# Optimization experiments

Measured on AMD Instinct MI355X. Metric: run time of the kernel, lower is better.

The kernel has to match this reference:

```python
import jax, jax.numpy as jnp
import numpy as np

QUERY_DIM, KEY_DIM, N_BATCH, N_KEYS = 512, 256, 2048, 512

def setup_inputs() -> dict:
    key = jax.random.key(0)
    k1, k2, k3, k4, k5, k6 = jax.random.split(key, 6)
    queries = jax.random.normal(k1, (N_BATCH, QUERY_DIM), dtype=jnp.float32)
    keys = jax.random.normal(k2, (N_BATCH, N_KEYS, KEY_DIM), dtype=jnp.float32)
    trans_keys = jax.random.normal(k3, (N_BATCH, N_KEYS, KEY_DIM), dtype=jnp.float32)
    null_mask = jax.random.randint(k4, (N_BATCH, N_KEYS), 0, 2).astype(jnp.bool_)
    # nn.Linear(query_dim, key_dim) params
    bound = 1.0 / np.sqrt(QUERY_DIM)
    W = jax.random.uniform(k5, (KEY_DIM, QUERY_DIM), dtype=jnp.float32, minval=-bound, maxval=bound)
    b = jax.random.uniform(k6, (KEY_DIM,), dtype=jnp.float32, minval=-bound, maxval=bound)
    return {"queries": queries, "keys": keys, "trans_keys": trans_keys,
            "null_mask": null_mask, "W": W, "b": b}

def reference(queries, keys, trans_keys, null_mask, W, b):
    # trans_queries = linear_in(queries): (B, key_dim)
    trans_queries = queries @ W.T + b
    # alpha = bmm(keys, trans_queries[:, :, None]).squeeze(2): (B, n_keys)
    alpha = jnp.einsum('bnk,bk->bn', keys, trans_queries)
    alpha = jnp.where(null_mask, -jnp.inf, alpha)
    alpha_sm = jax.nn.softmax(alpha, axis=1)
    # attened_keys = bmm(alpha_sm[:, None, :], keys).squeeze(1): (B, key_dim)
    attened_keys = jnp.einsum('bn,bnk->bk', alpha_sm, keys)
    return (attened_keys, alpha_sm)
```

## Files before the change

kernel.cpp:

```cpp
#include <hip/hip_runtime.h>
#include <stdint.h>

#define QD 512
#define KD 256
#define NBATCH 2048
#define NK 512

__global__ __launch_bounds__(256) void tq_gemm(const float* __restrict__ Q,
                                               const float* __restrict__ W,
                                               const float* __restrict__ bias,
                                               float* __restrict__ TQ) {
    __shared__ float qs[4][QD];
    const int b0 = blockIdx.x * 4;

    const float4* Qv = (const float4*)(Q + (size_t)b0 * QD);
    float4* qsv = (float4*)&qs[0][0];
    qsv[threadIdx.x]       = Qv[threadIdx.x];
    qsv[threadIdx.x + 256] = Qv[threadIdx.x + 256];
    __syncthreads();

    const int k = threadIdx.x;
    const float4* Wv = (const float4*)(W + (size_t)k * QD);

    float a0 = 0.f, a1 = 0.f, a2 = 0.f, a3 = 0.f;
#pragma unroll 4
    for (int kk = 0; kk < QD / 4; ++kk) {
        float4 w4 = Wv[kk];
        float4 q0 = *(const float4*)&qs[0][kk * 4];
        float4 q1 = *(const float4*)&qs[1][kk * 4];
        float4 q2 = *(const float4*)&qs[2][kk * 4];
        float4 q3 = *(const float4*)&qs[3][kk * 4];
        a0 += w4.x * q0.x + w4.y * q0.y + w4.z * q0.z + w4.w * q0.w;
        a1 += w4.x * q1.x + w4.y * q1.y + w4.z * q1.z + w4.w * q1.w;
        a2 += w4.x * q2.x + w4.y * q2.y + w4.z * q2.z + w4.w * q2.w;
        a3 += w4.x * q3.x + w4.y * q3.y + w4.z * q3.z + w4.w * q3.w;
    }
    const float bb = bias[k];
    TQ[(size_t)(b0 + 0) * KD + k] = a0 + bb;
    TQ[(size_t)(b0 + 1) * KD + k] = a1 + bb;
    TQ[(size_t)(b0 + 2) * KD + k] = a2 + bb;
    TQ[(size_t)(b0 + 3) * KD + k] = a3 + bb;
}

__global__ __launch_bounds__(256) void attn_fused(const float* __restrict__ keys,
                                                  const void* __restrict__ maskp,
                                                  const float* __restrict__ TQ,
                                                  float* __restrict__ out_att,
                                                  float* __restrict__ out_alpha) {
    const int b    = blockIdx.x;
    const int t    = threadIdx.x;
    const int wave = t >> 6;
    const int lane = t & 63;

    __shared__ float s_bias[NK];
    __shared__ float s_alpha[NK];
    __shared__ float s_acc[4][KD];
    __shared__ float s_m[4], s_l[4];
    __shared__ int   s_flag[4];

    const uint32_t* mw32 = (const uint32_t*)maskp + (size_t)b * NK;
    const uint32_t* mw8  = (const uint32_t*)((const uint8_t*)maskp + (size_t)b * NK);
    uint2 wv = ((const uint2*)mw32)[t];
    const bool big = (wv.x > 1u) | (wv.y > 1u);
    const unsigned long long bal = __ballot(big);
    if (lane == 0) s_flag[wave] = (bal != 0ull);
    __syncthreads();
    const int bytemask = s_flag[0] | s_flag[1] | s_flag[2] | s_flag[3];
    if (bytemask) {
        if (t < NK / 4) {
            uint32_t w = mw8[t];
            s_bias[4 * t + 0] = (w & 0x000000FFu) ? -INFINITY : 0.f;
            s_bias[4 * t + 1] = (w & 0x0000FF00u) ? -INFINITY : 0.f;
            s_bias[4 * t + 2] = (w & 0x00FF0000u) ? -INFINITY : 0.f;
            s_bias[4 * t + 3] = (w & 0xFF000000u) ? -INFINITY : 0.f;
        }
    } else {
        s_bias[2 * t + 0] = wv.x ? -INFINITY : 0.f;
        s_bias[2 * t + 1] = wv.y ? -INFINITY : 0.f;
    }
    __syncthreads();

    const float4 tq4 = *(const float4*)(TQ + (size_t)b * KD + lane * 4);
    const float* kb  = keys + (size_t)b * NK * KD;

    float m = -1e30f, l = 0.f;
    float ax = 0.f, ay = 0.f, az = 0.f, aw = 0.f;

    const int n0 = wave * (NK / 4);

    for (int i = 0; i < NK / 4; i += 8) {
        float4 k4[8];
#pragma unroll
        for (int r = 0; r < 8; ++r)
            k4[r] = *(const float4*)(kb + (size_t)(n0 + i + r) * KD + lane * 4);

#pragma unroll
        for (int r = 0; r < 8; ++r) {
            const int n = n0 + i + r;
            float d = k4[r].x * tq4.x + k4[r].y * tq4.y +
                      k4[r].z * tq4.z + k4[r].w * tq4.w;
#pragma unroll
            for (int off = 32; off > 0; off >>= 1)
                d += __shfl_xor(d, off, 64);

            const float aval = d + s_bias[n];
            if (lane == 0) s_alpha[n] = aval;

            if (aval > m) {
                const float sc = __expf(m - aval);
                l *= sc; ax *= sc; ay *= sc; az *= sc; aw *= sc;
                m = aval;
            }
            const float w = __expf(aval - m);
            l += w;
            ax += w * k4[r].x; ay += w * k4[r].y;
            az += w * k4[r].z; aw += w * k4[r].w;
        }
    }

    if (lane == 0) { s_m[wave] = m; s_l[wave] = l; }
    *(float4*)&s_acc[wave][lane * 4] = make_float4(ax, ay, az, aw);
    __syncthreads();

    const float M = fmaxf(fmaxf(s_m[0], s_m[1]), fmaxf(s_m[2], s_m[3]));
    const float sc0 = __expf(s_m[0] - M), sc1 = __expf(s_m[1] - M);
    const float sc2 = __expf(s_m[2] - M), sc3 = __expf(s_m[3] - M);
    const float L = s_l[0] * sc0 + s_l[1] * sc1 + s_l[2] * sc2 + s_l[3] * sc3;
    const float invL = 1.0f / L;

    const float o = (s_acc[0][t] * sc0 + s_acc[1][t] * sc1 +
                     s_acc[2][t] * sc2 + s_acc[3][t] * sc3) * invL;
    out_att[(size_t)b * KD + t] = o;

    out_alpha[(size_t)b * NK + t]       = __expf(s_alpha[t]       - M) * invL;
    out_alpha[(size_t)b * NK + t + 256] = __expf(s_alpha[t + 256] - M) * invL;
}

extern "C" void kernel_launch(void* const* d_in, const int* in_sizes, int n_in,
                              void* d_out, int out_size, void* d_ws, size_t ws_size,
                              hipStream_t stream) {
    const float* queries = (const float*)d_in[0];
    const float* keys    = (const float*)d_in[1];
    const void*  mask    = d_in[3];
    const float* W       = (const float*)d_in[4];
    const float* bias    = (const float*)d_in[5];

    float* out_att   = (float*)d_out;
    float* out_alpha = (float*)d_out + (size_t)NBATCH * KD;
    float* TQ        = (float*)d_ws;

    tq_gemm<<<NBATCH / 4, 256, 0, stream>>>(queries, W, bias, TQ);
    attn_fused<<<NBATCH, 256, 0, stream>>>(keys, mask, TQ, out_att, out_alpha);
}
```

Baseline: 246.8 us.

## Process four keys per wave with 16-lane groups and double-buffered loads

Each wave now splits into four 16-lane groups that each handle a different key row, so a dot product needs only a 4-step shuffle reduction instead of 6. A shared max is taken across the groups each step. Key loads are double-buffered across iterations to overlap memory with compute, and partial accumulators are reduced across groups at the end. The mask-format probe now reads only the first 128 words of the mask, which is a heuristic on the input data. The change also raises register use per thread.

```diff
diff --git a/kernel.cpp b/kernel.cpp
--- a/kernel.cpp
+++ b/kernel.cpp
@@ -51,6 +51,8 @@
     const int t    = threadIdx.x;
     const int wave = t >> 6;
     const int lane = t & 63;
+    const int grp  = lane >> 4;
+    const int sub  = lane & 15;
 
     __shared__ float s_bias[NK];
     __shared__ float s_alpha[NK];
@@ -58,68 +60,103 @@
     __shared__ float s_m[4], s_l[4];
     __shared__ int   s_flag[4];
 
-    const uint32_t* mw32 = (const uint32_t*)maskp + (size_t)b * NK;
-    const uint32_t* mw8  = (const uint32_t*)((const uint8_t*)maskp + (size_t)b * NK);
-    uint2 wv = ((const uint2*)mw32)[t];
-    const bool big = (wv.x > 1u) | (wv.y > 1u);
-    const unsigned long long bal = __ballot(big);
+    const uint32_t* mg = (const uint32_t*)maskp;
+    const uint32_t pv = (t < 128) ? mg[t] : 0u;
+    const unsigned long long bal = __ballot(pv > 1u);
     if (lane == 0) s_flag[wave] = (bal != 0ull);
     __syncthreads();
     const int bytemask = s_flag[0] | s_flag[1] | s_flag[2] | s_flag[3];
+
     if (bytemask) {
+        const uint32_t* mb8 = (const uint32_t*)((const uint8_t*)maskp + (size_t)b * NK);
         if (t < NK / 4) {
-            uint32_t w = mw8[t];
+            const uint32_t w = mb8[t];
             s_bias[4 * t + 0] = (w & 0x000000FFu) ? -INFINITY : 0.f;
             s_bias[4 * t + 1] = (w & 0x0000FF00u) ? -INFINITY : 0.f;
             s_bias[4 * t + 2] = (w & 0x00FF0000u) ? -INFINITY : 0.f;
             s_bias[4 * t + 3] = (w & 0xFF000000u) ? -INFINITY : 0.f;
         }
     } else {
+        const uint2 wv = ((const uint2*)((const uint32_t*)maskp + (size_t)b * NK))[t];
         s_bias[2 * t + 0] = wv.x ? -INFINITY : 0.f;
         s_bias[2 * t + 1] = wv.y ? -INFINITY : 0.f;
     }
     __syncthreads();
 
-    const float4 tq4 = *(const float4*)(TQ + (size_t)b * KD + lane * 4);
-    const float* kb  = keys + (size_t)b * NK * KD;
+    const float* tqb = TQ + (size_t)b * KD + sub * 4;
+    const float4 tq0 = *(const float4*)(tqb +   0);
+    const float4 tq1 = *(const float4*)(tqb +  64);
+    const float4 tq2 = *(const float4*)(tqb + 128);
+    const float4 tq3 = *(const float4*)(tqb + 192);
+
+    const int n0 = wave * (NK / 4);
+    const float* p = keys + (size_t)b * NK * KD + (size_t)(n0 + grp) * KD + sub * 4;
 
     float m = -1e30f, l = 0.f;
-    float ax = 0.f, ay = 0.f, az = 0.f, aw = 0.f;
+    float4 a0 = {0,0,0,0}, a1 = {0,0,0,0}, a2 = {0,0,0,0}, a3 = {0,0,0,0};
 
-    const int n0 = wave * (NK / 4);
+#define LOADG(i, K0, K1, K2, K3) do {                                   \
+    const float* q_ = p + (size_t)(i) * 4 * KD;                         \
+    K0 = *(const float4*)(q_ +   0);                                    \
+    K1 = *(const float4*)(q_ +  64);                                    \
+    K2 = *(const float4*)(q_ + 128);                                    \
+    K3 = *(const float4*)(q_ + 192);                                    \
+} while (0)
 
-    for (int i = 0; i < NK / 4; i += 8) {
-        float4 k4[8];
-#pragma unroll
-        for (int r = 0; r < 8; ++r)
-            k4[r] = *(const float4*)(kb + (size_t)(n0 + i + r) * KD + lane * 4);
+#define COMPUTE(i, K0, K1, K2, K3) do {                                 \
+    float d_ = K0.x*tq0.x + K0.y*tq0.y + K0.z*tq0.z + K0.w*tq0.w;       \
+    d_ += K1.x*tq1.x + K1.y*tq1.y + K1.z*tq1.z + K1.w*tq1.w;            \
+    d_ += K2.x*tq2.x + K2.y*tq2.y + K2.z*tq2.z + K2.w*tq2.w;            \
+    d_ += K3.x*tq3.x + K3.y*tq3.y + K3.z*tq3.z + K3.w*tq3.w;            \
+    d_ += __shfl_xor(d_, 8, 64);                                        \
+    d_ += __shfl_xor(d_, 4, 64);                                        \
+    d_ += __shfl_xor(d_, 2, 64);                                        \
+    d_ += __shfl_xor(d_, 1, 64);                                        \
+    const int n_ = n0 + 4 * (i) + grp;                                  \
+    const float aval_ = d_ + s_bias[n_];                                \
+    if (sub == 0) s_alpha[n_] = aval_;                                  \
+    float mx_ = fmaxf(aval_, __shfl_xor(aval_, 16, 64));                \
+    mx_ = fmaxf(mx_, __shfl_xor(mx_, 32, 64));                          \
+    if (mx_ > m) {       \
+        const float sc_ = __expf(m - mx_);                              \
+        l *= sc_;                                                       \
+        a0.x *= sc_; a0.y *= sc_; a0.z *= sc_; a0.w *= sc_;             \
+        a1.x *= sc_; a1.y *= sc_; a1.z *= sc_; a1.w *= sc_;             \
+        a2.x *= sc_; a2.y *= sc_; a2.z *= sc_; a2.w *= sc_;             \
+        a3.x *= sc_; a3.y *= sc_; a3.z *= sc_; a3.w *= sc_;             \
+        m = mx_;                                                        \
+    }                                                                   \
+    const float w_ = __expf(aval_ - m);   \
+    l += w_;                                                            \
+    a0.x += w_*K0.x; a0.y += w_*K0.y; a0.z += w_*K0.z; a0.w += w_*K0.w; \
+    a1.x += w_*K1.x; a1.y += w_*K1.y; a1.z += w_*K1.z; a1.w += w_*K1.w; \
+    a2.x += w_*K2.x; a2.y += w_*K2.y; a2.z += w_*K2.z; a2.w += w_*K2.w; \
+    a3.x += w_*K3.x; a3.y += w_*K3.y; a3.z += w_*K3.z; a3.w += w_*K3.w; \
+} while (0)
 
-#pragma unroll
-        for (int r = 0; r < 8; ++r) {
-            const int n = n0 + i + r;
-            float d = k4[r].x * tq4.x + k4[r].y * tq4.y +
-                      k4[r].z * tq4.z + k4[r].w * tq4.w;
-#pragma unroll
-            for (int off = 32; off > 0; off >>= 1)
-                d += __shfl_xor(d, off, 64);
-
-            const float aval = d + s_bias[n];
-            if (lane == 0) s_alpha[n] = aval;
-
-            if (aval > m) {
-                const float sc = __expf(m - aval);
-                l *= sc; ax *= sc; ay *= sc; az *= sc; aw *= sc;
-                m = aval;
-            }
-            const float w = __expf(aval - m);
-            l += w;
-            ax += w * k4[r].x; ay += w * k4[r].y;
-            az += w * k4[r].z; aw += w * k4[r].w;
-        }
+    float4 A0, A1, A2, A3, B0, B1, B2, B3;
+    LOADG(0, A0, A1, A2, A3);
+    for (int i = 0; i < 32; i += 2) {
+        LOADG(i + 1, B0, B1, B2, B3);
+        COMPUTE(i, A0, A1, A2, A3);
+        if (i + 2 < 32) LOADG(i + 2, A0, A1, A2, A3);
+        COMPUTE(i + 1, B0, B1, B2, B3);
     }
 
+#define RED2(x) do { x += __shfl_xor(x, 16, 64); x += __shfl_xor(x, 32, 64); } while (0)
+    RED2(l);
+    RED2(a0.x); RED2(a0.y); RED2(a0.z); RED2(a0.w);
+    RED2(a1.x); RED2(a1.y); RED2(a1.z); RED2(a1.w);
+    RED2(a2.x); RED2(a2.y); RED2(a2.z); RED2(a2.w);
+    RED2(a3.x); RED2(a3.y); RED2(a3.z); RED2(a3.w);
+
     if (lane == 0) { s_m[wave] = m; s_l[wave] = l; }
-    *(float4*)&s_acc[wave][lane * 4] = make_float4(ax, ay, az, aw);
+    float4 av;
+    av.x = grp == 0 ? a0.x : grp == 1 ? a1.x : grp == 2 ? a2.x : a3.x;
+    av.y = grp == 0 ? a0.y : grp == 1 ? a1.y : grp == 2 ? a2.y : a3.y;
+    av.z = grp == 0 ? a0.z : grp == 1 ? a1.z : grp == 2 ? a2.z : a3.z;
+    av.w = grp == 0 ? a0.w : grp == 1 ? a1.w : grp == 2 ? a2.w : a3.w;
+    *(float4*)&s_acc[wave][grp * 64 + sub * 4] = av;
     __syncthreads();
 
     const float M = fmaxf(fmaxf(s_m[0], s_m[1]), fmaxf(s_m[2], s_m[3]));
```

Result: faster. 236.9 us (-4.0%).
